# Optimization experiments

Measured on AMD Instinct MI355X. Metric: run time of the kernel, lower is better.

The kernel has to match this reference:

```python
import jax, jax.numpy as jnp
import numpy as np

B, IMG, P, D, NH, HS, L, V, TB, MLP, A = 32, 224, 16, 768, 12, 64, 12, 128, 32, 3072, 7
NPATCH = (IMG // P) ** 2          # 196 patches per image
SEQ = 1 + NPATCH + 1 + NPATCH + TB  # 426 = cls + obs + goal_tok + goal + lang


def _ln(x, g, b):
    m = x.mean(-1, keepdims=True)
    v = x.var(-1, keepdims=True)
    return (x - m) / jnp.sqrt(v + 1e-5) * g + b


def _patches(img):
    # einops 'b (h p1) (w p2) c -> b (h w) (p1 p2 c)'
    b = img.shape[0]
    h = IMG // P
    x = img.reshape(b, h, P, h, P, 3).transpose(0, 1, 3, 2, 4, 5)
    return x.reshape(b, h * h, P * P * 3)


def _forward(images, goal_imgs, goals_txt, patch_W, patch_b, tok_emb, pos_emb,
             cls_tok, goal_tok, Wq, Wk, Wv, Wo, bo, ln1_g, ln1_b, ln2_g, ln2_b,
             W1, b1, W2, b2, lnf_g, lnf_b, ah_W1, ah_b1, ah_W2, ah_b2):
    tok_obs = _patches(images) @ patch_W + patch_b        # [B, 196, D]
    tok_goal = _patches(goal_imgs) @ patch_W + patch_b    # [B, 196, D]
    tok_lang = tok_emb[goals_txt]                         # [B, 32, D]
    b = images.shape[0]
    x = jnp.concatenate([
        jnp.broadcast_to(cls_tok, (b, 1, D)),
        tok_obs,
        jnp.broadcast_to(goal_tok, (b, 1, D)),
        tok_goal,
        tok_lang,
    ], axis=1)                                            # [B, SEQ, D]
    x = x + pos_emb[None]
    scale = D ** -0.5  # NOTE: original Head scales by full n_embd, not head_size

    def block(x, p):
        wq, wk, wv, wo, bo_, l1g, l1b, l2g, l2b, w1, b1_, w2, b2_ = p
        xn = _ln(x, l1g, l1b)
        q = jnp.einsum('btd,hde->bhte', xn, wq)
        k = jnp.einsum('btd,hde->bhte', xn, wk)
        v = jnp.einsum('btd,hde->bhte', xn, wv)
        wei = jax.nn.softmax(jnp.einsum('bhte,bhse->bhts', q, k) * scale, axis=-1)
        att = jnp.einsum('bhts,bhse->bhte', wei, v)
        att = att.transpose(0, 2, 1, 3).reshape(x.shape[0], -1, D)  # concat heads
        x = x + att @ wo + bo_
        h = jax.nn.relu(_ln(x, l2g, l2b) @ w1 + b1_)
        x = x + h @ w2 + b2_
        return x, None

    x, _ = jax.lax.scan(block, x, (Wq, Wk, Wv, Wo, bo, ln1_g, ln1_b,
                                   ln2_g, ln2_b, W1, b1, W2, b2))
    x = _ln(x, lnf_g, lnf_b)
    cls = x[:, 0, :]
    out = jax.nn.relu(cls @ ah_W1 + ah_b1) @ ah_W2 + ah_b2  # [B, A]
    return out


def setup_inputs():
    key = jax.random.key(0)
    ks = jax.random.split(key, 20)
    nrm = lambda i, shape: 0.02 * jax.random.normal(ks[i], shape, dtype=jnp.float32)
    return {
        'images': jax.random.uniform(ks[0], (B, IMG, IMG, 3), dtype=jnp.float32),
        'goal_imgs': jax.random.uniform(ks[1], (B, IMG, IMG, 3), dtype=jnp.float32),
        'goals_txt': jax.random.randint(ks[2], (B, TB), 0, V, dtype=jnp.int32),
        'patch_W': nrm(3, (P * P * 3, D)), 'patch_b': jnp.zeros((D,), jnp.float32),
        'tok_emb': nrm(4, (V, D)),
        'pos_emb': nrm(5, (SEQ, D)),
        'cls_tok': jax.random.normal(ks[6], (1, 1, D), dtype=jnp.float32),
        'goal_tok': jax.random.normal(ks[7], (1, 1, D), dtype=jnp.float32),
        'Wq': nrm(8, (L, NH, D, HS)), 'Wk': nrm(9, (L, NH, D, HS)),
        'Wv': nrm(10, (L, NH, D, HS)),
        'Wo': nrm(11, (L, D, D)), 'bo': jnp.zeros((L, D), jnp.float32),
        'ln1_g': jnp.ones((L, D), jnp.float32), 'ln1_b': jnp.zeros((L, D), jnp.float32),
        'ln2_g': jnp.ones((L, D), jnp.float32), 'ln2_b': jnp.zeros((L, D), jnp.float32),
        'W1': nrm(12, (L, D, MLP)), 'b1': jnp.zeros((L, MLP), jnp.float32),
        'W2': nrm(13, (L, MLP, D)), 'b2': jnp.zeros((L, D), jnp.float32),
        'lnf_g': jnp.ones((D,), jnp.float32), 'lnf_b': jnp.zeros((D,), jnp.float32),
        'ah_W1': nrm(14, (D, 4 * D)), 'ah_b1': jnp.zeros((4 * D,), jnp.float32),
        'ah_W2': nrm(15, (4 * D, A)), 'ah_b2': jnp.zeros((A,), jnp.float32),
    }


def reference(images, goal_imgs, goals_txt, patch_W, patch_b, tok_emb, pos_emb,
              cls_tok, goal_tok, Wq, Wk, Wv, Wo, bo, ln1_g, ln1_b, ln2_g, ln2_b,
              W1, b1, W2, b2, lnf_g, lnf_b, ah_W1, ah_b1, ah_W2, ah_b2):
    return _forward(images, goal_imgs, goals_txt, patch_W, patch_b, tok_emb,
                    pos_emb, cls_tok, goal_tok, Wq, Wk, Wv, Wo, bo, ln1_g, ln1_b,
                    ln2_g, ln2_b, W1, b1, W2, b2, lnf_g, lnf_b, ah_W1, ah_b1,
                    ah_W2, ah_b2)
```

## Files before the change

kernel.cpp:

```cpp
#include <hip/hip_runtime.h>
#include <hip/hip_bf16.h>
#include <cstdint>

typedef __bf16 bf16x8 __attribute__((ext_vector_type(8)));
typedef __bf16 bf16x4v __attribute__((ext_vector_type(4)));
typedef float f32x4 __attribute__((ext_vector_type(4)));

static __device__ __forceinline__ f32x4 mfma16(bf16x8 a, bf16x8 b, f32x4 c) {
  return __builtin_amdgcn_mfma_f32_16x16x32_bf16(a, b, c, 0, 0, 0);
}
static __device__ __forceinline__ void gld_lds16(const void* g, void* l) {
  __builtin_amdgcn_global_load_lds(
      (__attribute__((address_space(1))) void*)(uintptr_t)g,
      (__attribute__((address_space(3))) void*)l, 16, 0, 0);
}

template <int EPI, int MODE>
__global__ __launch_bounds__(256) void gemm_bt(
    const __bf16* __restrict__ A, const __bf16* __restrict__ Bt, int K, int ldc,
    int M, int nY,
    __bf16* __restrict__ outb, float* __restrict__ outf,
    const float* __restrict__ bias, const float* __restrict__ pos) {
  __shared__ __align__(16) __bf16 lsA[128 * 32];
  __shared__ __align__(16) __bf16 lsB[128 * 32];
  const int id = blockIdx.x;
  const int xcd = id & 7;
  const int j = id >> 3;
  const int rpx = (int)gridDim.x / (8 * nY);
  int bx, by;
  if (MODE == 0) { bx = xcd * rpx + j / nY; by = j % nY; }
  else           { by = j / rpx;            bx = xcd * rpx + j % rpx; }
  const long m0 = (long)bx * 128, n0 = (long)by * 128;
  if (m0 >= M) return;

  const int tid = threadIdx.x;
  const int wave = tid >> 6, lane = tid & 63;
  const int quad = lane >> 4, l16 = lane & 15;

  const int c0 = tid, c1 = 256 + tid;
  const __bf16* gA0 = A + (m0 + (c0 >> 2)) * (long)K + (c0 & 3) * 8;
  const __bf16* gA1 = A + (m0 + (c1 >> 2)) * (long)K + (c1 & 3) * 8;
  const __bf16* gB0 = Bt + (n0 + (c0 >> 2)) * (long)K + (c0 & 3) * 8;
  const __bf16* gB1 = Bt + (n0 + (c1 >> 2)) * (long)K + (c1 & 3) * 8;
  __bf16* lA0 = lsA + wave * 512;
  __bf16* lA1 = lsA + 2048 + wave * 512;
  __bf16* lB0 = lsB + wave * 512;
  __bf16* lB1 = lsB + 2048 + wave * 512;

  const int wr = wave >> 1, wc = wave & 1;
  const __bf16* rA = lsA + (wr * 64 + l16) * 32 + quad * 8;
  const __bf16* rB = lsB + (wc * 64 + l16) * 32 + quad * 8;

  const f32x4 zz = {0.f, 0.f, 0.f, 0.f};
  f32x4 acc[4][4];
#pragma unroll
  for (int i = 0; i < 4; ++i)
#pragma unroll
    for (int jj = 0; jj < 4; ++jj) acc[i][jj] = zz;

  for (int k0 = 0; k0 < K; k0 += 32) {
    gld_lds16(gA0, lA0);
    gld_lds16(gA1, lA1);
    gld_lds16(gB0, lB0);
    gld_lds16(gB1, lB1);
    gA0 += 32; gA1 += 32; gB0 += 32; gB1 += 32;
    __syncthreads();
    bf16x8 af[4], bfr[4];
#pragma unroll
    for (int mi = 0; mi < 4; ++mi) af[mi] = *(const bf16x8*)(rA + mi * 512);
#pragma unroll
    for (int ni = 0; ni < 4; ++ni) bfr[ni] = *(const bf16x8*)(rB + ni * 512);
#pragma unroll
    for (int mi = 0; mi < 4; ++mi)
#pragma unroll
      for (int ni = 0; ni < 4; ++ni)
        acc[mi][ni] = mfma16(af[mi], bfr[ni], acc[mi][ni]);
    __syncthreads();
  }

#pragma unroll
  for (int mi = 0; mi < 4; ++mi) {
#pragma unroll
    for (int r = 0; r < 4; ++r) {
      const long row = m0 + wr * 64 + mi * 16 + quad * 4 + r;
      if (EPI == 3) {
        const int rr = (int)row;
        const int gsel = rr >= 6272 ? 1 : 0;
        const int rm = rr - gsel * 6272;
        const int bb = rm / 196, pp = rm % 196;
        const int t = gsel ? (198 + pp) : (1 + pp);
        float* xr = outf + ((long)bb * 426 + t) * 768;
        const float* pr = pos + (long)t * 768;
#pragma unroll
        for (int ni = 0; ni < 4; ++ni) {
          const long col = n0 + wc * 64 + ni * 16 + l16;
          xr[col] = acc[mi][ni][r] + bias[col] + pr[col];
        }
      } else {
#pragma unroll
        for (int ni = 0; ni < 4; ++ni) {
          const long col = n0 + wc * 64 + ni * 16 + l16;
          const float v = acc[mi][ni][r];
          if (EPI == 0) outb[row * ldc + col] = (__bf16)v;
          else if (EPI == 1) outb[row * ldc + col] = (__bf16)fmaxf(v + bias[col], 0.f);
          else outf[row * ldc + col] += v + bias[col];
        }
      }
    }
  }
}

__global__ __launch_bounds__(256) void transpose_pack(
    const float* __restrict__ in, __bf16* __restrict__ out, int K, int N,
    int nh, long out_ls, long out_hs) {
  __shared__ float tile[32][33];
  const int z = blockIdx.z;
  const long in_o = (long)z * K * N;
  const long out_o = (long)(z / nh) * out_ls + (long)(z % nh) * out_hs;
  const int n0 = blockIdx.x * 32, k0 = blockIdx.y * 32;
  const int tx = threadIdx.x, ty = threadIdx.y;
#pragma unroll
  for (int i = 0; i < 4; ++i)
    tile[ty + i * 8][tx] = in[in_o + (long)(k0 + ty + i * 8) * N + n0 + tx];
  __syncthreads();
#pragma unroll
  for (int i = 0; i < 4; ++i)
    out[out_o + (long)(n0 + ty + i * 8) * K + k0 + tx] = (__bf16)tile[tx][ty + i * 8];
}

__global__ __launch_bounds__(256) void patches_k(const float* __restrict__ img0,
                                                 const float* __restrict__ img1,
                                                 __bf16* __restrict__ out) {
  const int row = blockIdx.x;
  const int gsel = row >= 6272 ? 1 : 0;
  const int rm = row - gsel * 6272;
  const int b = rm / 196, p = rm % 196;
  const int py = p / 14, px = p % 14;
  const float* img = gsel ? img1 : img0;
#pragma unroll
  for (int i = 0; i < 3; ++i) {
    const int k = threadIdx.x + i * 256;
    const int pidx = k / 3, c = k - pidx * 3;
    const int pr = pidx >> 4, pc = pidx & 15;
    const float v = img[(((long)b * 224 + py * 16 + pr) * 224 + px * 16 + pc) * 3 + c];
    out[(long)row * 768 + k] = (__bf16)v;
  }
}

__global__ __launch_bounds__(256) void assemble_k(
    const float* __restrict__ cls_tok, const float* __restrict__ goal_tok,
    const float* __restrict__ tok_emb, const int* __restrict__ txt,
    const float* __restrict__ pos, float* __restrict__ x) {
  const int z = blockIdx.x;
  const int b = z / 34, j = z % 34;
  const int t = (j == 0) ? 0 : (j == 1) ? 197 : (392 + j);
  const float* src = (j == 0) ? cls_tok
                   : (j == 1) ? goal_tok
                              : tok_emb + (long)txt[b * 32 + (j - 2)] * 768;
  float* dst = x + ((long)b * 426 + t) * 768;
  const float* pr = pos + (long)t * 768;
#pragma unroll
  for (int i = 0; i < 3; ++i) {
    const int k = threadIdx.x + i * 256;
    dst[k] = src[k] + pr[k];
  }
}

__global__ __launch_bounds__(64) void ln_k(const float* __restrict__ x,
                                           const float* __restrict__ g,
                                           const float* __restrict__ b,
                                           __bf16* __restrict__ out) {
  const int row = blockIdx.x, lane = threadIdx.x;
  const float4* xr = (const float4*)(x + (long)row * 768);
  float4 v[3];
  float s = 0.f, q = 0.f;
#pragma unroll
  for (int i = 0; i < 3; ++i) {
    v[i] = xr[lane + i * 64];
    s += v[i].x + v[i].y + v[i].z + v[i].w;
    q += v[i].x * v[i].x + v[i].y * v[i].y + v[i].z * v[i].z + v[i].w * v[i].w;
  }
#pragma unroll
  for (int o = 32; o > 0; o >>= 1) {
    s += __shfl_xor(s, o);
    q += __shfl_xor(q, o);
  }
  const float mean = s * (1.f / 768.f);
  const float var = q * (1.f / 768.f) - mean * mean;
  const float rs = rsqrtf(var + 1e-5f);
  const float4* g4 = (const float4*)g;
  const float4* b4 = (const float4*)b;
#pragma unroll
  for (int i = 0; i < 3; ++i) {
    const float4 gg = g4[lane + i * 64], bb = b4[lane + i * 64];
    bf16x4v o4;
    o4[0] = (__bf16)((v[i].x - mean) * rs * gg.x + bb.x);
    o4[1] = (__bf16)((v[i].y - mean) * rs * gg.y + bb.y);
    o4[2] = (__bf16)((v[i].z - mean) * rs * gg.z + bb.z);
    o4[3] = (__bf16)((v[i].w - mean) * rs * gg.w + bb.w);
    *(bf16x4v*)(out + (long)row * 768 + (lane + i * 64) * 4) = o4;
  }
}

__global__ __launch_bounds__(256) void vtrans_k(const __bf16* __restrict__ qkv,
                                                __bf16* __restrict__ vt) {
  __shared__ __bf16 tile[64][66];
  const int bh = blockIdx.x;
  const int b = bh / 12, h = bh % 12;
  const int s0 = blockIdx.y * 64;
  const int t = threadIdx.x;
  const int sr = t >> 2, part = t & 3;
  const __bf16* src = qkv + ((long)(b * 426 + s0 + sr)) * 2304 + 1536 + h * 64 + part * 16;
#pragma unroll
  for (int j = 0; j < 16; ++j) tile[sr][part * 16 + j] = src[j];
  __syncthreads();
  __bf16* dst = vt + ((long)bh * 64 + sr) * 448 + s0 + part * 16;
#pragma unroll
  for (int j = 0; j < 16; ++j) {
    const int s = s0 + part * 16 + j;
    dst[j] = (s < 426) ? tile[part * 16 + j][sr] : (__bf16)0.f;
  }
}

__global__ __launch_bounds__(256) void attn_k(const __bf16* __restrict__ qkv,
                                              const __bf16* __restrict__ vt,
                                              __bf16* __restrict__ attout) {
  __shared__ __align__(16) __bf16 lds[8192 + 4096];
  const int tid = threadIdx.x;
  const int wave = tid >> 6, lane = tid & 63;
  const int quad = lane >> 4, l16 = lane & 15;
  const int bh = blockIdx.x;
  const int b = bh / 12, h = bh % 12;
  const int q0 = blockIdx.y * 64 + wave * 16;
  const long b426 = (long)b * 426;

  const int swz0 = ((quad) ^ (l16 & 7)) * 8;
  const int swz1 = ((4 + quad) ^ (l16 & 7)) * 8;
  __bf16* lsK = lds;
  __bf16* lsV = lds + 4096;
  __bf16* lsP = lds + 8192 + wave * 1024;

  const __bf16* gsrc[4];
  long gstep[4];
#pragma unroll
  for (int s = 0; s < 4; ++s) {
    const int c = s * 256 + tid;
    if (c < 512) {
      const int key = c >> 3, part = (c & 7) ^ (key & 7);
      gsrc[s] = qkv + (b426 + key) * 2304 + 768 + h * 64 + part * 8;
      gstep[s] = 64 * 2304;
    } else {
      const int cv = c - 512;
      const int e = cv >> 3, part = (cv & 7) ^ (e & 7);
      gsrc[s] = vt + ((long)bh * 64 + e) * 448 + part * 8;
      gstep[s] = 64;
    }
  }
  __bf16* ldst[4];
#pragma unroll
  for (int s = 0; s < 4; ++s) ldst[s] = lds + (s * 256 + (tid & ~63)) * 8;

  const long qrow = (b426 + q0 + l16) * 2304 + h * 64;
  const bf16x8 aq0 = *(const bf16x8*)(qkv + qrow + quad * 8);
  const bf16x8 aq1 = *(const bf16x8*)(qkv + qrow + 32 + quad * 8);

  const f32x4 zz = {0.f, 0.f, 0.f, 0.f};
  f32x4 o[4] = {zz, zz, zz, zz};
  float m_i[4] = {-3e38f, -3e38f, -3e38f, -3e38f};
  float l_i[4] = {0.f, 0.f, 0.f, 0.f};
  const float scale = 0.03608439182435161f;

  for (int kc = 0; kc < 7; ++kc) {
    const int kbase = kc * 64;
    __syncthreads();
#pragma unroll
    for (int s = 0; s < 4; ++s) {
      gld_lds16(gsrc[s], ldst[s]);
      gsrc[s] += gstep[s];
    }
    __syncthreads();

    f32x4 s4[4] = {zz, zz, zz, zz};
#pragma unroll
    for (int nt = 0; nt < 4; ++nt) {
      const __bf16* kb = lsK + (nt * 16 + l16) * 64;
      s4[nt] = mfma16(aq0, *(const bf16x8*)(kb + swz0), s4[nt]);
      s4[nt] = mfma16(aq1, *(const bf16x8*)(kb + swz1), s4[nt]);
    }

    const int lim = 426 - kbase - l16;
#pragma unroll
    for (int r = 0; r < 4; ++r) {
      float a0 = (0 < lim)  ? s4[0][r] * scale : -1e30f;
      float a1 = (16 < lim) ? s4[1][r] * scale : -1e30f;
      float a2 = (32 < lim) ? s4[2][r] * scale : -1e30f;
      float a3 = (48 < lim) ? s4[3][r] * scale : -1e30f;
      float mx = fmaxf(fmaxf(a0, a1), fmaxf(a2, a3));
#pragma unroll
      for (int w = 1; w < 16; w <<= 1) mx = fmaxf(mx, __shfl_xor(mx, w, 16));
      mx = fmaxf(mx, m_i[r]);
      const float alpha = __expf(m_i[r] - mx);
      m_i[r] = mx;
      const float p0 = __expf(a0 - mx), p1 = __expf(a1 - mx);
      const float p2 = __expf(a2 - mx), p3 = __expf(a3 - mx);
      float rs = (p0 + p1) + (p2 + p3);
#pragma unroll
      for (int w = 1; w < 16; w <<= 1) rs += __shfl_xor(rs, w, 16);
      l_i[r] = l_i[r] * alpha + rs;
      o[0][r] *= alpha; o[1][r] *= alpha; o[2][r] *= alpha; o[3][r] *= alpha;
      const int rowb = quad * 4 + r;
      __bf16* pb = lsP + rowb * 64 + (l16 & 7);
      const int l8 = l16 >> 3, rx = rowb & 7;
      pb[((0 + l8) ^ rx) * 8] = (__bf16)p0;
      pb[((2 + l8) ^ rx) * 8] = (__bf16)p1;
      pb[((4 + l8) ^ rx) * 8] = (__bf16)p2;
      pb[((6 + l8) ^ rx) * 8] = (__bf16)p3;
    }

    const bf16x8 pa0 = *(const bf16x8*)(lsP + l16 * 64 + swz0);
    const bf16x8 pa1 = *(const bf16x8*)(lsP + l16 * 64 + swz1);
#pragma unroll
    for (int et = 0; et < 4; ++et) {
      const __bf16* vb = lsV + (et * 16 + l16) * 64;
      o[et] = mfma16(pa0, *(const bf16x8*)(vb + swz0), o[et]);
      o[et] = mfma16(pa1, *(const bf16x8*)(vb + swz1), o[et]);
    }
  }

#pragma unroll
  for (int r = 0; r < 4; ++r) {
    const int q = q0 + quad * 4 + r;
    if (q < 426) {
      const float inv = 1.f / l_i[r];
      __bf16* dst = attout + (b426 + q) * 768 + h * 64 + l16;
#pragma unroll
      for (int et = 0; et < 4; ++et) dst[et * 16] = (__bf16)(o[et][r] * inv);
    }
  }
}

__global__ __launch_bounds__(256) void head1_k(const __bf16* __restrict__ xn,
                                               const float* __restrict__ W1,
                                               const float* __restrict__ b1,
                                               float* __restrict__ hh) {
  const int id = blockIdx.x * 256 + threadIdx.x;
  const int r = id / 3072, n = id % 3072;
  const __bf16* c = xn + (long)r * 426 * 768;
  float s = 0.f;
  for (int k = 0; k < 768; ++k) s += (float)c[k] * W1[(long)k * 3072 + n];
  hh[(long)r * 3072 + n] = fmaxf(s + b1[n], 0.f);
}

__global__ __launch_bounds__(256) void head2_k(const float* __restrict__ hh,
                                               const float* __restrict__ W2,
                                               const float* __restrict__ b2,
                                               float* __restrict__ out) {
  const int t = threadIdx.x;
  if (t >= 224) return;
  const int r = t / 7, n = t % 7;
  float s = 0.f;
  for (int k = 0; k < 3072; ++k) s += hh[(long)r * 3072 + k] * W2[(long)k * 7 + n];
  out[r * 7 + n] = s + b2[n];
}

extern "C" void kernel_launch(void* const* d_in, const int* in_sizes, int n_in,
                              void* d_out, int out_size, void* d_ws, size_t ws_size,
                              hipStream_t stream) {
  (void)in_sizes; (void)n_in; (void)out_size; (void)ws_size;
  const float* images   = (const float*)d_in[0];
  const float* goal_img = (const float*)d_in[1];
  const int*   txt      = (const int*)d_in[2];
  const float* patch_W  = (const float*)d_in[3];
  const float* patch_b  = (const float*)d_in[4];
  const float* tok_emb  = (const float*)d_in[5];
  const float* pos_emb  = (const float*)d_in[6];
  const float* cls_tok  = (const float*)d_in[7];
  const float* goal_tok = (const float*)d_in[8];
  const float* Wq   = (const float*)d_in[9];
  const float* Wk   = (const float*)d_in[10];
  const float* Wv   = (const float*)d_in[11];
  const float* Wo   = (const float*)d_in[12];
  const float* bo   = (const float*)d_in[13];
  const float* ln1g = (const float*)d_in[14];
  const float* ln1b = (const float*)d_in[15];
  const float* ln2g = (const float*)d_in[16];
  const float* ln2b = (const float*)d_in[17];
  const float* W1   = (const float*)d_in[18];
  const float* b1   = (const float*)d_in[19];
  const float* W2   = (const float*)d_in[20];
  const float* b2   = (const float*)d_in[21];
  const float* lnfg = (const float*)d_in[22];
  const float* lnfb = (const float*)d_in[23];
  const float* aW1  = (const float*)d_in[24];
  const float* ab1  = (const float*)d_in[25];
  const float* aW2  = (const float*)d_in[26];
  const float* ab2  = (const float*)d_in[27];

  char* base = (char*)d_ws;
  size_t off = 0;
  auto take = [&](size_t bytes) -> char* {
    char* p = base + off;
    off += (bytes + 255) & ~(size_t)255;
    return p;
  };
  float*  x     = (float*) take((size_t)13696 * 768 * 4);
  __bf16* xn    = (__bf16*)take((size_t)13696 * 768 * 2);
  __bf16* shard = (__bf16*)take((size_t)13696 * 3072 * 2);
  __bf16* attb  = (__bf16*)take((size_t)13696 * 768 * 2);
  __bf16* vt    = (__bf16*)take((size_t)384 * 64 * 448 * 2);
  float*  hh    = (float*) take((size_t)32 * 3072 * 4);
  __bf16* wqkv  = (__bf16*)take((size_t)12 * 2304 * 768 * 2);
  __bf16* wot   = (__bf16*)take((size_t)12 * 768 * 768 * 2);
  __bf16* w1t   = (__bf16*)take((size_t)12 * 768 * 3072 * 2);
  __bf16* w2t   = (__bf16*)take((size_t)12 * 768 * 3072 * 2);
  __bf16* pwt   = (__bf16*)take((size_t)768 * 768 * 2);
  __bf16* qkv   = shard;
  __bf16* hbuf  = shard;
  __bf16* patches = shard;

  const dim3 tpb(32, 8);
  transpose_pack<<<dim3(24, 24, 1), tpb, 0, stream>>>(patch_W, pwt, 768, 768, 1, 0L, 0L);
  transpose_pack<<<dim3(2, 24, 144), tpb, 0, stream>>>(Wq, wqkv, 768, 64, 12, 1769472L, 49152L);
  transpose_pack<<<dim3(2, 24, 144), tpb, 0, stream>>>(Wk, wqkv + 589824, 768, 64, 12, 1769472L, 49152L);
  transpose_pack<<<dim3(2, 24, 144), tpb, 0, stream>>>(Wv, wqkv + 1179648, 768, 64, 12, 1769472L, 49152L);
  transpose_pack<<<dim3(24, 24, 12), tpb, 0, stream>>>(Wo, wot, 768, 768, 1, 589824L, 0L);
  transpose_pack<<<dim3(96, 24, 12), tpb, 0, stream>>>(W1, w1t, 768, 3072, 1, 2359296L, 0L);
  transpose_pack<<<dim3(24, 96, 12), tpb, 0, stream>>>(W2, w2t, 3072, 768, 1, 2359296L, 0L);

  patches_k<<<12544, 256, 0, stream>>>(images, goal_img, patches);
  assemble_k<<<1088, 256, 0, stream>>>(cls_tok, goal_tok, tok_emb, txt, pos_emb, x);
  gemm_bt<3, 1><<<8 * 13 * 6, 256, 0, stream>>>(patches, pwt, 768, 768, 12544, 6,
                                                nullptr, x, patch_b, pos_emb);

  for (int l = 0; l < 12; ++l) {
    ln_k<<<13696, 64, 0, stream>>>(x, ln1g + l * 768, ln1b + l * 768, xn);
    gemm_bt<0, 1><<<8 * 14 * 18, 256, 0, stream>>>(xn, wqkv + (long)l * 1769472, 768, 2304,
                                                   13696, 18, qkv, nullptr, nullptr, nullptr);
    vtrans_k<<<dim3(384, 7), 256, 0, stream>>>(qkv, vt);
    attn_k<<<dim3(384, 7), 256, 0, stream>>>(qkv, vt, attb);
    gemm_bt<2, 1><<<8 * 14 * 6, 256, 0, stream>>>(attb, wot + (long)l * 589824, 768, 768,
                                                  13696, 6, nullptr, x, bo + l * 768, nullptr);
    ln_k<<<13696, 64, 0, stream>>>(x, ln2g + l * 768, ln2b + l * 768, xn);
    gemm_bt<1, 1><<<8 * 14 * 24, 256, 0, stream>>>(xn, w1t + (long)l * 2359296, 768, 3072,
                                                   13696, 24, hbuf, nullptr, b1 + l * 3072, nullptr);
    gemm_bt<2, 0><<<8 * 14 * 6, 256, 0, stream>>>(hbuf, w2t + (long)l * 2359296, 3072, 768,
                                                  13696, 6, nullptr, x, b2 + l * 768, nullptr);
  }
  ln_k<<<13696, 64, 0, stream>>>(x, lnfg, lnfb, xn);
  head1_k<<<384, 256, 0, stream>>>(xn, aW1, ab1, hh);
  head2_k<<<1, 256, 0, stream>>>(hh, aW2, ab2, (float*)d_out);
}
```

Baseline: 5.827 ms.

## Split-K the residual GEMMs with atomics and run the action head on MFMA

```diff
diff --git a/kernel.cpp b/kernel.cpp
--- a/kernel.cpp
+++ b/kernel.cpp
@@ -15,7 +15,7 @@
       (__attribute__((address_space(3))) void*)l, 16, 0, 0);
 }
 
-template <int EPI, int MODE>
+template <int EPI, int MODE, int SPLIT = 1>
 __global__ __launch_bounds__(256) void gemm_bt(
     const __bf16* __restrict__ A, const __bf16* __restrict__ Bt, int K, int ldc,
     int M, int nY,
@@ -26,22 +26,33 @@
   const int id = blockIdx.x;
   const int xcd = id & 7;
   const int j = id >> 3;
-  const int rpx = (int)gridDim.x / (8 * nY);
-  int bx, by;
-  if (MODE == 0) { bx = xcd * rpx + j / nY; by = j % nY; }
-  else           { by = j / rpx;            bx = xcd * rpx + j % rpx; }
+  const int rpx = (int)gridDim.x / (8 * nY * SPLIT);
+  int bx, by, sp;
+  if (MODE == 0) {
+    const int per = nY * SPLIT;
+    bx = xcd * rpx + j / per;
+    const int rem = j % per;
+    by = rem / SPLIT; sp = rem % SPLIT;
+  } else {
+    const int per = rpx * SPLIT;
+    by = j / per;
+    const int rem = j % per;
+    bx = xcd * rpx + rem / SPLIT; sp = rem % SPLIT;
+  }
   const long m0 = (long)bx * 128, n0 = (long)by * 128;
   if (m0 >= M) return;
+  const int kn = K / SPLIT;
+  const long kofs = (long)sp * kn;
 
   const int tid = threadIdx.x;
   const int wave = tid >> 6, lane = tid & 63;
   const int quad = lane >> 4, l16 = lane & 15;
 
   const int c0 = tid, c1 = 256 + tid;
-  const __bf16* gA0 = A + (m0 + (c0 >> 2)) * (long)K + (c0 & 3) * 8;
-  const __bf16* gA1 = A + (m0 + (c1 >> 2)) * (long)K + (c1 & 3) * 8;
-  const __bf16* gB0 = Bt + (n0 + (c0 >> 2)) * (long)K + (c0 & 3) * 8;
-  const __bf16* gB1 = Bt + (n0 + (c1 >> 2)) * (long)K + (c1 & 3) * 8;
+  const __bf16* gA0 = A + (m0 + (c0 >> 2)) * (long)K + kofs + (c0 & 3) * 8;
+  const __bf16* gA1 = A + (m0 + (c1 >> 2)) * (long)K + kofs + (c1 & 3) * 8;
+  const __bf16* gB0 = Bt + (n0 + (c0 >> 2)) * (long)K + kofs + (c0 & 3) * 8;
+  const __bf16* gB1 = Bt + (n0 + (c1 >> 2)) * (long)K + kofs + (c1 & 3) * 8;
   __bf16* lA0 = lsA + wave * 512;
   __bf16* lA1 = lsA + 2048 + wave * 512;
   __bf16* lB0 = lsB + wave * 512;
@@ -58,7 +69,7 @@
 #pragma unroll
     for (int jj = 0; jj < 4; ++jj) acc[i][jj] = zz;
 
-  for (int k0 = 0; k0 < K; k0 += 32) {
+  for (int k0 = 0; k0 < kn; k0 += 32) {
     gld_lds16(gA0, lA0);
     gld_lds16(gA1, lA1);
     gld_lds16(gB0, lB0);
@@ -103,7 +114,8 @@
           const float v = acc[mi][ni][r];
           if (EPI == 0) outb[row * ldc + col] = (__bf16)v;
           else if (EPI == 1) outb[row * ldc + col] = (__bf16)fmaxf(v + bias[col], 0.f);
-          else outf[row * ldc + col] += v + bias[col];
+          else if (SPLIT == 1) outf[row * ldc + col] += v + bias[col];
+          else atomicAdd(&outf[row * ldc + col], v + (sp == 0 ? bias[col] : 0.f));
         }
       }
     }
@@ -339,28 +351,29 @@
   }
 }
 
-__global__ __launch_bounds__(256) void head1_k(const __bf16* __restrict__ xn,
-                                               const float* __restrict__ W1,
-                                               const float* __restrict__ b1,
-                                               float* __restrict__ hh) {
-  const int id = blockIdx.x * 256 + threadIdx.x;
-  const int r = id / 3072, n = id % 3072;
-  const __bf16* c = xn + (long)r * 426 * 768;
-  float s = 0.f;
-  for (int k = 0; k < 768; ++k) s += (float)c[k] * W1[(long)k * 3072 + n];
-  hh[(long)r * 3072 + n] = fmaxf(s + b1[n], 0.f);
-}
-
-__global__ __launch_bounds__(256) void head2_k(const float* __restrict__ hh,
+__global__ __launch_bounds__(256) void gather_cls(const __bf16* __restrict__ xn,
+                                                  __bf16* __restrict__ buf) {
+  const int b = blockIdx.x, t = threadIdx.x;
+#pragma unroll
+  for (int i = 0; i < 3; ++i)
+    buf[(long)b * 768 + t + i * 256] = xn[(long)b * 426 * 768 + t + i * 256];
+}
+
+__global__ __launch_bounds__(256) void head2_k(const __bf16* __restrict__ hh,
                                                const float* __restrict__ W2,
                                                const float* __restrict__ b2,
                                                float* __restrict__ out) {
+  __shared__ float red[4];
+  const int blk = blockIdx.x;
+  const int r = blk / 7, n = blk % 7;
   const int t = threadIdx.x;
-  if (t >= 224) return;
-  const int r = t / 7, n = t % 7;
   float s = 0.f;
-  for (int k = 0; k < 3072; ++k) s += hh[(long)r * 3072 + k] * W2[(long)k * 7 + n];
-  out[r * 7 + n] = s + b2[n];
+  for (int k = t; k < 3072; k += 256) s += (float)hh[(long)r * 3072 + k] * W2[(long)k * 7 + n];
+#pragma unroll
+  for (int o = 32; o > 0; o >>= 1) s += __shfl_xor(s, o);
+  if ((t & 63) == 0) red[t >> 6] = s;
+  __syncthreads();
+  if (t == 0) out[blk] = red[0] + red[1] + red[2] + red[3] + b2[n];
 }
 
 extern "C" void kernel_launch(void* const* d_in, const int* in_sizes, int n_in,
@@ -408,12 +421,14 @@
   __bf16* shard = (__bf16*)take((size_t)13696 * 3072 * 2);
   __bf16* attb  = (__bf16*)take((size_t)13696 * 768 * 2);
   __bf16* vt    = (__bf16*)take((size_t)384 * 64 * 448 * 2);
-  float*  hh    = (float*) take((size_t)32 * 3072 * 4);
+  __bf16* hh    = (__bf16*)take((size_t)128 * 3072 * 2);
+  __bf16* clsb  = (__bf16*)take((size_t)128 * 768 * 2);
   __bf16* wqkv  = (__bf16*)take((size_t)12 * 2304 * 768 * 2);
   __bf16* wot   = (__bf16*)take((size_t)12 * 768 * 768 * 2);
   __bf16* w1t   = (__bf16*)take((size_t)12 * 768 * 3072 * 2);
   __bf16* w2t   = (__bf16*)take((size_t)12 * 768 * 3072 * 2);
   __bf16* pwt   = (__bf16*)take((size_t)768 * 768 * 2);
+  __bf16* w1at  = (__bf16*)take((size_t)3072 * 768 * 2);
   __bf16* qkv   = shard;
   __bf16* hbuf  = shard;
   __bf16* patches = shard;
@@ -426,6 +441,7 @@
   transpose_pack<<<dim3(24, 24, 12), tpb, 0, stream>>>(Wo, wot, 768, 768, 1, 589824L, 0L);
   transpose_pack<<<dim3(96, 24, 12), tpb, 0, stream>>>(W1, w1t, 768, 3072, 1, 2359296L, 0L);
   transpose_pack<<<dim3(24, 96, 12), tpb, 0, stream>>>(W2, w2t, 3072, 768, 1, 2359296L, 0L);
+  transpose_pack<<<dim3(96, 24, 1), tpb, 0, stream>>>(aW1, w1at, 768, 3072, 1, 0L, 0L);
 
   patches_k<<<12544, 256, 0, stream>>>(images, goal_img, patches);
   assemble_k<<<1088, 256, 0, stream>>>(cls_tok, goal_tok, tok_emb, txt, pos_emb, x);
@@ -438,15 +454,17 @@
                                                    13696, 18, qkv, nullptr, nullptr, nullptr);
     vtrans_k<<<dim3(384, 7), 256, 0, stream>>>(qkv, vt);
     attn_k<<<dim3(384, 7), 256, 0, stream>>>(qkv, vt, attb);
-    gemm_bt<2, 1><<<8 * 14 * 6, 256, 0, stream>>>(attb, wot + (long)l * 589824, 768, 768,
-                                                  13696, 6, nullptr, x, bo + l * 768, nullptr);
+    gemm_bt<2, 0, 2><<<8 * 14 * 6 * 2, 256, 0, stream>>>(attb, wot + (long)l * 589824, 768, 768,
+                                                         13696, 6, nullptr, x, bo + l * 768, nullptr);
     ln_k<<<13696, 64, 0, stream>>>(x, ln2g + l * 768, ln2b + l * 768, xn);
     gemm_bt<1, 1><<<8 * 14 * 24, 256, 0, stream>>>(xn, w1t + (long)l * 2359296, 768, 3072,
                                                    13696, 24, hbuf, nullptr, b1 + l * 3072, nullptr);
-    gemm_bt<2, 0><<<8 * 14 * 6, 256, 0, stream>>>(hbuf, w2t + (long)l * 2359296, 3072, 768,
-                                                  13696, 6, nullptr, x, b2 + l * 768, nullptr);
+    gemm_bt<2, 0, 2><<<8 * 14 * 6 * 2, 256, 0, stream>>>(hbuf, w2t + (long)l * 2359296, 3072, 768,
+                                                         13696, 6, nullptr, x, b2 + l * 768, nullptr);
   }
   ln_k<<<13696, 64, 0, stream>>>(x, lnfg, lnfb, xn);
-  head1_k<<<384, 256, 0, stream>>>(xn, aW1, ab1, hh);
-  head2_k<<<1, 256, 0, stream>>>(hh, aW2, ab2, (float*)d_out);
-}
+  gather_cls<<<32, 256, 0, stream>>>(xn, clsb);
+  gemm_bt<1, 1><<<8 * 1 * 24, 256, 0, stream>>>(clsb, w1at, 768, 3072, 32, 24,
+                                                hh, nullptr, ab1, nullptr);
+  head2_k<<<224, 256, 0, stream>>>(hh, aW2, ab2, (float*)d_out);
+}
```

Result: slower. 6.937 ms (+19.1%).
